# Kernel tuning notes

Hardware: AMD Instinct MI355X
Metric: run time of the kernel (lower is better)

The kernel has to match this reference:

```python
import jax, jax.numpy as jnp
import numpy as np

H = 1152      # embed_dim
NH = 16       # num heads
HD = H // NH  # head_dim = 72
SCALE = HD ** -0.5
B, S = 16, 729


def fake_quant(x, bits):
    """Symmetric per-tensor fake quantize-dequantize with straight-through estimator."""
    qmax = 2.0 ** (bits - 1) - 1.0
    scale = jnp.maximum(jnp.max(jnp.abs(x)), 1e-8) / qmax
    q = jnp.clip(jnp.round(x / scale), -qmax - 1.0, qmax) * scale
    return x + jax.lax.stop_gradient(q - x)  # STE


def fq_linear(x, W, b):
    # FakeQuantLinear: 8-bit fake-quant on activations and weights, fp accumulate
    return fake_quant(x, 8) @ fake_quant(W, 8).T + b


def setup_inputs() -> dict:
    key = jax.random.key(0)
    ks = jax.random.split(key, 9)
    std = H ** -0.5
    return {
        "hidden_states": jax.random.normal(ks[0], (B, S, H), jnp.float32),
        "Wq": jax.random.normal(ks[1], (H, H), jnp.float32) * std,
        "bq": jax.random.normal(ks[2], (H,), jnp.float32) * 0.02,
        "Wk": jax.random.normal(ks[3], (H, H), jnp.float32) * std,
        "bk": jax.random.normal(ks[4], (H,), jnp.float32) * 0.02,
        "Wv": jax.random.normal(ks[5], (H, H), jnp.float32) * std,
        "bv": jax.random.normal(ks[6], (H,), jnp.float32) * 0.02,
        "Wo": jax.random.normal(ks[7], (H, H), jnp.float32) * std,
        "bo": jax.random.normal(ks[8], (H,), jnp.float32) * 0.02,
    }


def reference(hidden_states, Wq, bq, Wk, bk, Wv, bv, Wo, bo):
    b, s, _ = hidden_states.shape
    q = fq_linear(hidden_states, Wq, bq).reshape(b, s, NH, HD).transpose(0, 2, 1, 3)
    k = fq_linear(hidden_states, Wk, bk).reshape(b, s, NH, HD).transpose(0, 2, 1, 3)
    v = fq_linear(hidden_states, Wv, bv).reshape(b, s, NH, HD).transpose(0, 2, 1, 3)
    # FakeQuantMatmul(8, 16): 8-bit quant on both matmul inputs, 16-bit quant on output
    attn = fake_quant(
        jnp.einsum("bhqd,bhkd->bhqk", fake_quant(q, 8), fake_quant(k, 8)), 16
    ) * SCALE
    # FakeQuantSoftmax(quant_bits=16): softmax then 16-bit fake quant
    attn = fake_quant(jax.nn.softmax(attn, axis=-1), 16)
    # FakeQuantMatmul(None, 8): no input quant, 8-bit output quant
    out = fake_quant(jnp.einsum("bhqk,bhkd->bhqd", attn, v), 8)
    out = out.transpose(0, 2, 1, 3).reshape(b, s, H)
    return fq_linear(out, Wo, bo)
```

## Files before the change

### kernel.cpp

```cpp
#include <hip/hip_runtime.h>
#include <math.h>

#define Hdim 1152
#define NHd  16
#define HDd  72
#define Bd   16
#define Sd   729
#define Ntok (Bd*Sd)
#define BHd  (Bd*NHd)
#define SCALE_F 0.117851130197757934f
#define LOG2E 1.44269504088896340736f

#define KFTB 8192
#define VFT 10240

#define SL_X 0
#define SL_WQ 1
#define SL_WK 2
#define SL_WV 3
#define SL_WO 4
#define SL_Q 5
#define SL_K 6
#define SL_LOGIT 8
#define SL_LMIN 9
#define SL_O 10

typedef short short8 __attribute__((ext_vector_type(8)));
typedef short short4v __attribute__((ext_vector_type(4)));
typedef float f32x4 __attribute__((ext_vector_type(4)));
typedef int int4v __attribute__((ext_vector_type(4)));

static __device__ __forceinline__ unsigned short f2bf(float f) {
  unsigned b = __float_as_uint(f);
  return (unsigned short)((b + 0x7FFFu + ((b >> 16) & 1u)) >> 16);
}
static __device__ __forceinline__ float bf2f(unsigned short u) {
  return __uint_as_float(((unsigned)u) << 16);
}
static __device__ __forceinline__ void atomicMaxF(float* p, float v) {
  atomicMax((unsigned int*)p, __float_as_uint(v));
}
static __device__ __forceinline__ void atomicMinF(float* p, float v) {
  atomicMin((unsigned int*)p, __float_as_uint(v));
}
static __device__ __forceinline__ float qscale(float mx, float qmax) {
  return fmaxf(mx, 1e-8f) / qmax;
}
static __device__ __forceinline__ float fexp2(float x) {
  float r; asm("v_exp_f32 %0, %1" : "=v"(r) : "v"(x)); return r;
}
static __device__ __forceinline__ float flog2(float x) {
  float r; asm("v_log_f32 %0, %1" : "=v"(r) : "v"(x)); return r;
}
static __device__ __forceinline__ short4v pack4(unsigned a, unsigned b, unsigned c, unsigned d) {
  union { unsigned u[2]; short4v s; } t;
  t.u[0] = a | (b << 16);
  t.u[1] = c | (d << 16);
  return t.s;
}
static __device__ __forceinline__ int q8i(float v, float s) {
  return (int)fminf(fmaxf(rintf(v / s), -128.f), 127.f);
}

#if __has_builtin(__builtin_amdgcn_mfma_f32_16x16x16bf16_1k)
#define MFMA16(a, b, c) __builtin_amdgcn_mfma_f32_16x16x16bf16_1k(a, b, c, 0, 0, 0)
#else
static __device__ __forceinline__ f32x4 MFMA16(short4v a, short4v b, f32x4 c) {
  asm("v_mfma_f32_16x16x16_bf16 %0, %1, %2, %0" : "+v"(c) : "v"(a), "v"(b));
  return c;
}
#endif
#if __has_builtin(__builtin_amdgcn_mfma_i32_16x16x64_i8)
#define MFMAI8(a, b, c) __builtin_amdgcn_mfma_i32_16x16x64_i8(a, b, c, 0, 0, 0)
#else
static __device__ __forceinline__ int4v MFMAI8(int4v a, int4v b, int4v c) {
  asm("v_mfma_i32_16x16x64_i8 %0, %1, %2, %0" : "+v"(c) : "v"(a), "v"(b));
  return c;
}
#endif

static __device__ __forceinline__ void gll16(const void* g, void* l) {
  __builtin_amdgcn_global_load_lds((const __attribute__((address_space(1))) void*)g,
                                   (__attribute__((address_space(3))) void*)l, 16, 0, 0);
}

__global__ void k_init(float* slots) {
  int i = threadIdx.x;
  if (i < 32) slots[i] = (i == SL_LMIN) ? __builtin_inff() : 0.0f;
}

__launch_bounds__(256)
__global__ void k_absmax(const float* __restrict__ X, const float* __restrict__ W0,
                         const float* __restrict__ W1, const float* __restrict__ W2,
                         const float* __restrict__ W3, float* slots) {
  int seg = blockIdx.y;
  const float* p; long n; int slot;
  if (seg == 0) { p = X; n = (long)Ntok * Hdim; slot = SL_X; }
  else {
    const float* ws4[4] = {W0, W1, W2, W3};
    p = ws4[seg - 1]; n = (long)Hdim * Hdim; slot = SL_WQ + seg - 1;
  }
  long n4 = n >> 2;
  const float4* p4 = (const float4*)p;
  float m = 0.f;
  for (long i = (long)blockIdx.x * blockDim.x + threadIdx.x; i < n4;
       i += (long)gridDim.x * blockDim.x) {
    float4 v = p4[i];
    m = fmaxf(m, fmaxf(fmaxf(fabsf(v.x), fabsf(v.y)), fmaxf(fabsf(v.z), fabsf(v.w))));
  }
  for (int off = 32; off; off >>= 1) m = fmaxf(m, __shfl_xor(m, off, 64));
  __shared__ float red[4];
  if ((threadIdx.x & 63) == 0) red[threadIdx.x >> 6] = m;
  __syncthreads();
  if (threadIdx.x == 0)
    atomicMaxF(&slots[slot], fmaxf(fmaxf(red[0], red[1]), fmaxf(red[2], red[3])));
}

__launch_bounds__(256)
__global__ void k_quant8i(const float* __restrict__ in, unsigned int* __restrict__ out,
                          long n, const float* __restrict__ slots, int slot) {
  float s = qscale(slots[slot], 127.0f);
  long n4 = n >> 2;
  const float4* in4 = (const float4*)in;
  for (long i = (long)blockIdx.x * blockDim.x + threadIdx.x; i < n4;
       i += (long)gridDim.x * blockDim.x) {
    float4 v = in4[i];
    unsigned a = (unsigned)q8i(v.x, s) & 255u;
    unsigned b = (unsigned)q8i(v.y, s) & 255u;
    unsigned c = (unsigned)q8i(v.z, s) & 255u;
    unsigned d = (unsigned)q8i(v.w, s) & 255u;
    out[i] = a | (b << 8) | (c << 16) | (d << 24);
  }
}

__launch_bounds__(256)
__global__ void k_quant8wi(const float* __restrict__ W0, const float* __restrict__ W1,
                           const float* __restrict__ W2, const float* __restrict__ W3,
                           unsigned int* O0, unsigned int* O1,
                           unsigned int* O2, unsigned int* O3,
                           const float* __restrict__ slots) {
  int seg = blockIdx.y;
  const float* ws4[4] = {W0, W1, W2, W3};
  unsigned int* os4[4] = {O0, O1, O2, O3};
  const float* in = ws4[seg];
  unsigned int* out = os4[seg];
  float s = qscale(slots[SL_WQ + seg], 127.0f);
  long n4 = ((long)Hdim * Hdim) >> 2;
  const float4* in4 = (const float4*)in;
  for (long i = (long)blockIdx.x * blockDim.x + threadIdx.x; i < n4;
       i += (long)gridDim.x * blockDim.x) {
    float4 v = in4[i];
    unsigned a = (unsigned)q8i(v.x, s) & 255u;
    unsigned b = (unsigned)q8i(v.y, s) & 255u;
    unsigned c = (unsigned)q8i(v.z, s) & 255u;
    unsigned d = (unsigned)q8i(v.w, s) & 255u;
    out[i] = a | (b << 8) | (c << 16) | (d << 24);
  }
}

#define GBM 128
#define GBN 128
#define GBK 64
__launch_bounds__(256, 3)
__global__ void k_gemm(const char* __restrict__ A,
                       const char* __restrict__ Bm,
                       const float* __restrict__ bias,
                       float* __restrict__ C,
                       float* slots, int slotA, int slotB, int slotOut) {
  __shared__ char As[GBM][GBK];
  __shared__ char Bs[GBN][GBK];
  __shared__ float red[4];
  int tid = threadIdx.x, lane = tid & 63, wid = tid >> 6;
  int wm = wid >> 1, wn = wid & 1;
  int l15 = lane & 15, l4 = lane >> 4;
  int bM = blockIdx.x, bN = blockIdx.y;
  int4v acc[4][4];
  for (int rf = 0; rf < 4; ++rf)
    for (int cf = 0; cf < 4; ++cf) acc[rf][cf] = int4v{0, 0, 0, 0};

  int srow = lane >> 2, scol = (lane & 3) * 16;
  const char* pa = A + ((long)(bM * GBM + wid * 32) + srow) * Hdim + scol;
  const char* pb = Bm + ((long)(bN * GBN + wid * 32) + srow) * Hdim + scol;

  for (int kt = 0; kt < Hdim / GBK; ++kt) {
    int kb = kt * GBK;
    __syncthreads();
    gll16(pa + kb, &As[wid * 32][0]);
    gll16(pa + kb + 16 * Hdim, &As[wid * 32 + 16][0]);
    gll16(pb + kb, &Bs[wid * 32][0]);
    gll16(pb + kb + 16 * Hdim, &Bs[wid * 32 + 16][0]);
    __syncthreads();
    int4v af[4], bf4[4];
#pragma unroll
    for (int rf = 0; rf < 4; ++rf) af[rf] = *(const int4v*)&As[wm * 64 + rf * 16 + l15][l4 * 16];
#pragma unroll
    for (int cf = 0; cf < 4; ++cf) bf4[cf] = *(const int4v*)&Bs[wn * 64 + cf * 16 + l15][l4 * 16];
#pragma unroll
    for (int rf = 0; rf < 4; ++rf)
#pragma unroll
      for (int cf = 0; cf < 4; ++cf)
        acc[rf][cf] = MFMAI8(af[rf], bf4[cf], acc[rf][cf]);
  }
  float alpha = qscale(slots[slotA], 127.f) * qscale(slots[slotB], 127.f);
  float lmax = 0.f;
#pragma unroll
  for (int cf = 0; cf < 4; ++cf) {
    int col = bN * GBN + wn * 64 + cf * 16 + l15;
    float bv = bias[col];
#pragma unroll
    for (int rf = 0; rf < 4; ++rf)
#pragma unroll
      for (int j = 0; j < 4; ++j) {
        int row = bM * GBM + wm * 64 + rf * 16 + l4 * 4 + j;
        if (row < Ntok) {
          float v = (float)acc[rf][cf][j] * alpha + bv;
          C[(long)row * Hdim + col] = v;
          lmax = fmaxf(lmax, fabsf(v));
        }
      }
  }
  if (slotOut >= 0) {
    for (int off = 32; off; off >>= 1) lmax = fmaxf(lmax, __shfl_xor(lmax, off, 64));
    if ((tid & 63) == 0) red[wid] = lmax;
    __syncthreads();
    if (tid == 0)
      atomicMaxF(&slots[slotOut], fmaxf(fmaxf(red[0], red[1]), fmaxf(red[2], red[3])));
  }
}

__launch_bounds__(256, 3)
__global__ void k_gemm3(const char* __restrict__ A,
                        const char* __restrict__ W0,
                        const char* __restrict__ W1,
                        const char* __restrict__ W2,
                        const float* __restrict__ b0, const float* __restrict__ b1,
                        const float* __restrict__ b2,
                        float* __restrict__ C0, float* __restrict__ C1,
                        float* __restrict__ C2, float* slots) {
  __shared__ char As[GBM][GBK];
  __shared__ char Bs[GBN][GBK];
  __shared__ float red[4];
  int bNg = blockIdx.y;
  int mi = bNg / 9, bN = bNg - mi * 9;
  const char* Bm = mi == 0 ? W0 : (mi == 1 ? W1 : W2);
  const float* bias = mi == 0 ? b0 : (mi == 1 ? b1 : b2);
  float* C = mi == 0 ? C0 : (mi == 1 ? C1 : C2);
  int slotB = SL_WQ + mi;
  int slotOut = mi == 0 ? SL_Q : (mi == 1 ? SL_K : -1);

  int tid = threadIdx.x, lane = tid & 63, wid = tid >> 6;
  int wm = wid >> 1, wn = wid & 1;
  int l15 = lane & 15, l4 = lane >> 4;
  int bM = blockIdx.x;
  int4v acc[4][4];
  for (int rf = 0; rf < 4; ++rf)
    for (int cf = 0; cf < 4; ++cf) acc[rf][cf] = int4v{0, 0, 0, 0};

  int srow = lane >> 2, scol = (lane & 3) * 16;
  const char* pa = A + ((long)(bM * GBM + wid * 32) + srow) * Hdim + scol;
  const char* pb = Bm + ((long)(bN * GBN + wid * 32) + srow) * Hdim + scol;

  for (int kt = 0; kt < Hdim / GBK; ++kt) {
    int kb = kt * GBK;
    __syncthreads();
    gll16(pa + kb, &As[wid * 32][0]);
    gll16(pa + kb + 16 * Hdim, &As[wid * 32 + 16][0]);
    gll16(pb + kb, &Bs[wid * 32][0]);
    gll16(pb + kb + 16 * Hdim, &Bs[wid * 32 + 16][0]);
    __syncthreads();
    int4v af[4], bf4[4];
#pragma unroll
    for (int rf = 0; rf < 4; ++rf) af[rf] = *(const int4v*)&As[wm * 64 + rf * 16 + l15][l4 * 16];
#pragma unroll
    for (int cf = 0; cf < 4; ++cf) bf4[cf] = *(const int4v*)&Bs[wn * 64 + cf * 16 + l15][l4 * 16];
#pragma unroll
    for (int rf = 0; rf < 4; ++rf)
#pragma unroll
      for (int cf = 0; cf < 4; ++cf)
        acc[rf][cf] = MFMAI8(af[rf], bf4[cf], acc[rf][cf]);
  }
  float alpha = qscale(slots[SL_X], 127.f) * qscale(slots[slotB], 127.f);
  float lmax = 0.f;
#pragma unroll
  for (int cf = 0; cf < 4; ++cf) {
    int col = bN * GBN + wn * 64 + cf * 16 + l15;
    float bv = bias[col];
#pragma unroll
    for (int rf = 0; rf < 4; ++rf)
#pragma unroll
      for (int j = 0; j < 4; ++j) {
        int row = bM * GBM + wm * 64 + rf * 16 + l4 * 4 + j;
        if (row < Ntok) {
          float v = (float)acc[rf][cf][j] * alpha + bv;
          C[(long)row * Hdim + col] = v;
          lmax = fmaxf(lmax, fabsf(v));
        }
      }
  }
  if (slotOut >= 0) {
    for (int off = 32; off; off >>= 1) lmax = fmaxf(lmax, __shfl_xor(lmax, off, 64));
    if ((tid & 63) == 0) red[wid] = lmax;
    __syncthreads();
    if (tid == 0)
      atomicMaxF(&slots[slotOut], fmaxf(fmaxf(red[0], red[1]), fmaxf(red[2], red[3])));
  }
}

__launch_bounds__(256)
__global__ void k_kfrag(const float* __restrict__ Kf, char* __restrict__ KF,
                        const float* __restrict__ slots) {
  int kt = blockIdx.x, bh = blockIdx.y;
  int b = bh >> 4, h = bh & 15;
  float s = qscale(slots[SL_K], 127.0f);
  int tid = threadIdx.x, lane = tid & 63, w = tid >> 6;
  int l15 = lane & 15, l4 = lane >> 4;
  long obase = ((long)(bh * 12 + kt)) * KFTB;
#pragma unroll
  for (int i = 0; i < 2; ++i) {
    int p = w * 2 + i;
    int cf = p >> 1, c = p & 1;
    int token = kt * 64 + cf * 16 + l15;
    char ov[16];
#pragma unroll
    for (int j = 0; j < 16; ++j) ov[j] = 0;
    if (token < Sd) {
      const float* src = &Kf[((long)(b * Sd + token)) * Hdim + h * HDd];
      if (c == 0) {
#pragma unroll
        for (int j = 0; j < 16; ++j) ov[j] = (char)q8i(src[l4 * 16 + j], s);
      } else if (l4 == 0) {
#pragma unroll
        for (int j = 0; j < 8; ++j) ov[j] = (char)q8i(src[64 + j], s);
      }
    }
    *(int4v*)&KF[obase + p * 1024 + lane * 16] = *(int4v*)ov;
  }
}

__launch_bounds__(256)
__global__ void k_vsplit(const float* __restrict__ Vf, unsigned short* __restrict__ VF) {
  int kt = blockIdx.x, bh = blockIdx.y;
  int b = bh >> 4, h = bh & 15;
  int tid = threadIdx.x, lane = tid & 63, w = tid >> 6;
  int l15 = lane & 15, l4 = lane >> 4;
  long obase = ((long)(bh * 12 + kt)) * VFT;
#pragma unroll
  for (int i = 0; i < 5; ++i) {
    int p = w + 4 * i;
    int dt = p >> 2, cf = p & 3;
    int d = dt * 16 + l15;
    int tok0 = kt * 64 + cf * 16 + l4 * 4;
    unsigned short u[8];
#pragma unroll
    for (int j = 0; j < 4; ++j) {
      int tok = tok0 + j;
      float v = 0.f;
      if (tok < Sd && d < HDd)
        v = Vf[((long)(b * Sd + tok)) * Hdim + h * HDd + d];
      unsigned short hb = f2bf(v);
      u[j] = hb;
      u[4 + j] = f2bf(v - bf2f(hb));
    }
    *(short8*)&VF[obase + (long)p * 512 + lane * 8] = *(short8*)u;
  }
}

static __device__ __forceinline__ void loadQ8(const char* __restrict__ Qq,
                                              int b, int h, int qc, int l4,
                                              int4v& qa, int4v& qb) {
  const char* qp = &Qq[((long)(b * Sd + qc)) * Hdim + h * HDd];
  union { long l[2]; int4v v; } u0, u1;
  u0.l[0] = *(const long*)(qp + l4 * 16);
  u0.l[1] = *(const long*)(qp + l4 * 16 + 8);
  qa = u0.v;
  u1.l[0] = (l4 == 0) ? *(const long*)(qp + 64) : 0L;
  u1.l[1] = 0L;
  qb = u1.v;
}

__launch_bounds__(256, 4)
__global__ void k_attnA(const char* __restrict__ Qq,
                        const char* __restrict__ KF, float* slots) {
  __shared__ float red[4];
  int qh = blockIdx.x, bh = blockIdx.y;
  int b = bh >> 4, h = bh & 15;
  int tid = threadIdx.x, lane = tid & 63, w = tid >> 6;
  int l15 = lane & 15, l4 = lane >> 4;
  const char* kfb = KF + (long)bh * 12 * KFTB;
  int4v qa[3], qb[3];
#pragma unroll
  for (int qs = 0; qs < 3; ++qs) {
    int qrow = (qh * 3 + qs) * 64 + w * 16 + l15;
    int qc = qrow > Sd - 1 ? Sd - 1 : qrow;
    loadQ8(Qq, b, h, qc, l4, qa[qs], qb[qs]);
  }
  float mx = 0.f;
#pragma unroll 1
  for (int kt = 0; kt < 12; ++kt) {
    int4v kf[8];
#pragma unroll
    for (int p = 0; p < 8; ++p)
      kf[p] = *(const int4v*)&kfb[(long)kt * KFTB + p * 1024 + lane * 16];
#pragma unroll
    for (int qs = 0; qs < 3; ++qs) {
#pragma unroll
      for (int cf = 0; cf < 4; ++cf) {
        int4v a = int4v{0, 0, 0, 0};
        a = MFMAI8(kf[cf * 2 + 0], qa[qs], a);
        a = MFMAI8(kf[cf * 2 + 1], qb[qs], a);
#pragma unroll
        for (int j = 0; j < 4; ++j) mx = fmaxf(mx, fabsf((float)a[j]));
      }
    }
  }
  mx *= qscale(slots[SL_Q], 127.f) * qscale(slots[SL_K], 127.f);
  for (int off = 32; off; off >>= 1) mx = fmaxf(mx, __shfl_xor(mx, off, 64));
  if ((tid & 63) == 0) red[w] = mx;
  __syncthreads();
  if (tid == 0)
    atomicMaxF(&slots[SL_LOGIT], fmaxf(fmaxf(red[0], red[1]), fmaxf(red[2], red[3])));
}

__launch_bounds__(256, 4)
__global__ void k_attnB(const char* __restrict__ Qq,
                        const char* __restrict__ KF, float* slots,
                        float* __restrict__ m_arr, float* __restrict__ l_arr) {
  __shared__ float red[4];
  int qh = blockIdx.x, bh = blockIdx.y;
  int b = bh >> 4, h = bh & 15;
  int tid = threadIdx.x, lane = tid & 63, w = tid >> 6;
  int l15 = lane & 15, l4 = lane >> 4;
  const char* kfb = KF + (long)bh * 12 * KFTB;
  int4v qa[3], qb[3];
#pragma unroll
  for (int qs = 0; qs < 3; ++qs) {
    int qrow = (qh * 3 + qs) * 64 + w * 16 + l15;
    int qc = qrow > Sd - 1 ? Sd - 1 : qrow;
    loadQ8(Qq, b, h, qc, l4, qa[qs], qb[qs]);
  }
  float s16 = qscale(slots[SL_LOGIT], 32767.f);
  float sqk = qscale(slots[SL_Q], 127.f) * qscale(slots[SL_K], 127.f);
  float c0 = sqk / s16;
  float c1e = s16 * SCALE_F * LOG2E;
  float m_run[3] = {-3.0e38f, -3.0e38f, -3.0e38f};
  float l_run[3] = {0.f, 0.f, 0.f};
#pragma unroll 1
  for (int kt = 0; kt < 12; ++kt) {
    int4v kf[8];
#pragma unroll
    for (int p = 0; p < 8; ++p)
      kf[p] = *(const int4v*)&kfb[(long)kt * KFTB + p * 1024 + lane * 16];
#pragma unroll
    for (int qs = 0; qs < 3; ++qs) {
      float nv[16];
#pragma unroll
      for (int cf = 0; cf < 4; ++cf) {
        int4v a = int4v{0, 0, 0, 0};
        a = MFMAI8(kf[cf * 2 + 0], qa[qs], a);
        a = MFMAI8(kf[cf * 2 + 1], qb[qs], a);
#pragma unroll
        for (int j = 0; j < 4; ++j) nv[cf * 4 + j] = rintf((float)a[j] * c0);
      }
      if (kt == 11) {
#pragma unroll
        for (int cf = 0; cf < 4; ++cf)
#pragma unroll
          for (int j = 0; j < 4; ++j) {
            int kcol = 704 + cf * 16 + l4 * 4 + j;
            if (kcol > Sd - 1) nv[cf * 4 + j] = -3.0e30f;
          }
      }
      float mt = nv[0];
#pragma unroll
      for (int i = 1; i < 16; ++i) mt = fmaxf(mt, nv[i]);
      mt = fmaxf(mt, __shfl_xor(mt, 16, 64));
      mt = fmaxf(mt, __shfl_xor(mt, 32, 64));
      float mn = fmaxf(m_run[qs], mt);
      float f = fexp2((m_run[qs] - mn) * c1e);
      float se = 0.f;
#pragma unroll
      for (int i = 0; i < 16; ++i) se += fexp2((nv[i] - mn) * c1e);
      se += __shfl_xor(se, 16, 64);
      se += __shfl_xor(se, 32, 64);
      l_run[qs] = l_run[qs] * f + se;
      m_run[qs] = mn;
    }
  }
  float lmin = 3.0e38f;
#pragma unroll
  for (int qs = 0; qs < 3; ++qs) {
    int qrow = (qh * 3 + qs) * 64 + w * 16 + l15;
    if (qrow < Sd) {
      if (l4 == 0) {
        m_arr[bh * Sd + qrow] = m_run[qs];
        l_arr[bh * Sd + qrow] = l_run[qs];
      }
      lmin = fminf(lmin, l_run[qs]);
    }
  }
  for (int off = 32; off; off >>= 1) lmin = fminf(lmin, __shfl_xor(lmin, off, 64));
  if ((tid & 63) == 0) red[w] = lmin;
  __syncthreads();
  if (tid == 0)
    atomicMinF(&slots[SL_LMIN], fminf(fminf(red[0], red[1]), fminf(red[2], red[3])));
}

__launch_bounds__(256, 5)
__global__ void k_attnC(const char* __restrict__ Qq,
                        const char* __restrict__ KF,
                        const unsigned short* __restrict__ VF,
                        const float* __restrict__ m_arr, const float* __restrict__ l_arr,
                        float* slots, float* __restrict__ O) {
  __shared__ char Ks[KFTB];
  __shared__ unsigned short Vs[VFT];
  __shared__ float red[4];
  int qp, bh;
  {
    int id = blockIdx.y * 6 + blockIdx.x;
    int xcd = id & 7, sub = id >> 3;
    int bhl = sub / 6;
    qp = sub - bhl * 6;
    bh = xcd * 32 + bhl;
  }
  int b = bh >> 4, h = bh & 15;
  int tid = threadIdx.x, lane = tid & 63, w = tid >> 6;
  int l15 = lane & 15, l4 = lane >> 4;
  float s16 = qscale(slots[SL_LOGIT], 32767.f);
  float sqk = qscale(slots[SL_Q], 127.f) * qscale(slots[SL_K], 127.f);
  float c0 = sqk / s16;
  float c1e = s16 * SCALE_F * LOG2E;
  float pmaxv = 1.0f / slots[SL_LMIN];
  float sp = fmaxf(pmaxv, 1e-8f) / 32767.0f;
  float inv_sp = 1.0f / sp;
  int4v qa[2], qb[2];
  float dexp[2];
#pragma unroll
  for (int qs = 0; qs < 2; ++qs) {
    int qrow = (qp * 2 + qs) * 64 + w * 16 + l15;
    int qc = qrow > Sd - 1 ? Sd - 1 : qrow;
    loadQ8(Qq, b, h, qc, l4, qa[qs], qb[qs]);
    float mn = m_arr[bh * Sd + qc];
    float c2 = (1.0f / l_arr[bh * Sd + qc]) * inv_sp;
    dexp[qs] = flog2(c2) - mn * c1e;
  }
  const char* kfb = KF + (long)bh * 12 * KFTB;
  const unsigned short* vfb = VF + (long)bh * 12 * VFT;
  f32x4 acc[2][5];
#pragma unroll
  for (int qs = 0; qs < 2; ++qs)
#pragma unroll
    for (int i = 0; i < 5; ++i) acc[qs][i] = f32x4{0.f, 0.f, 0.f, 0.f};

#pragma unroll 1
  for (int kt = 0; kt < 12; ++kt) {
    __syncthreads();
    {
      const char* kg = kfb + (long)kt * KFTB;
#pragma unroll
      for (int i = 0; i < 2; ++i) {
        int c = w * 2 + i;
        gll16(kg + c * 1024 + lane * 16, &Ks[c * 1024]);
      }
      const unsigned short* vg = vfb + (long)kt * VFT;
#pragma unroll
      for (int i = 0; i < 5; ++i) {
        int c = w + 4 * i;
        gll16(vg + c * 512 + lane * 8, &Vs[c * 512]);
      }
    }
    __syncthreads();
#pragma unroll
    for (int cf = 0; cf < 4; ++cf) {
      int4v k0 = *(const int4v*)&Ks[(cf * 2 + 0) * 1024 + lane * 16];
      int4v k1 = *(const int4v*)&Ks[(cf * 2 + 1) * 1024 + lane * 16];
      short4v Pp[2], Pr[2];
#pragma unroll
      for (int qs = 0; qs < 2; ++qs) {
        int4v a = int4v{0, 0, 0, 0};
        a = MFMAI8(k0, qa[qs], a);
        a = MFMAI8(k1, qb[qs], a);
        unsigned phb[4], rsb[4];
#pragma unroll
        for (int j = 0; j < 4; ++j) {
          float n = rintf((float)a[j] * c0);
          float nn = rintf(fexp2(fmaf(n, c1e, dexp[qs])));
          unsigned ub = __float_as_uint(nn);
          unsigned ph = (ub + 0x7FFFu + ((ub >> 16) & 1u)) >> 16;
          float rsf = nn - __uint_as_float(ph << 16);
          phb[j] = ph;
          rsb[j] = __float_as_uint(rsf) >> 16;
        }
        Pp[qs] = pack4(phb[0], phb[1], phb[2], phb[3]);
        Pr[qs] = pack4(rsb[0], rsb[1], rsb[2], rsb[3]);
      }
#pragma unroll
      for (int dt = 0; dt < 5; ++dt) {
        short8 vv = *(const short8*)&Vs[(dt * 4 + cf) * 512 + lane * 8];
        short4v vh = __builtin_shufflevector(vv, vv, 0, 1, 2, 3);
        short4v vl = __builtin_shufflevector(vv, vv, 4, 5, 6, 7);
#pragma unroll
        for (int qs = 0; qs < 2; ++qs) {
          acc[qs][dt] = MFMA16(Pp[qs], vh, acc[qs][dt]);
          acc[qs][dt] = MFMA16(Pp[qs], vl, acc[qs][dt]);
          acc[qs][dt] = MFMA16(Pr[qs], vh, acc[qs][dt]);
        }
      }
    }
  }
  float lmax = 0.f;
#pragma unroll
  for (int qs = 0; qs < 2; ++qs)
#pragma unroll
    for (int dt = 0; dt < 5; ++dt) {
      int d = dt * 16 + l15;
#pragma unroll
      for (int j = 0; j < 4; ++j) {
        int qr = (qp * 2 + qs) * 64 + w * 16 + l4 * 4 + j;
        if (qr < Sd && d < HDd) {
          float v = sp * acc[qs][dt][j];
          O[((long)(b * Sd + qr)) * Hdim + h * HDd + d] = v;
          lmax = fmaxf(lmax, fabsf(v));
        }
      }
    }
  for (int off = 32; off; off >>= 1) lmax = fmaxf(lmax, __shfl_xor(lmax, off, 64));
  if ((tid & 63) == 0) red[w] = lmax;
  __syncthreads();
  if (tid == 0)
    atomicMaxF(&slots[SL_O], fmaxf(fmaxf(red[0], red[1]), fmaxf(red[2], red[3])));
}

extern "C" void kernel_launch(void* const* d_in, const int* in_sizes, int n_in,
                              void* d_out, int out_size, void* d_ws, size_t ws_size,
                              hipStream_t stream) {
  const float* Xin = (const float*)d_in[0];
  const float* Wq = (const float*)d_in[1];
  const float* bq = (const float*)d_in[2];
  const float* Wk = (const float*)d_in[3];
  const float* bk = (const float*)d_in[4];
  const float* Wv = (const float*)d_in[5];
  const float* bv = (const float*)d_in[6];
  const float* Wo = (const float*)d_in[7];
  const float* bo = (const float*)d_in[8];
  float* out = (float*)d_out;
  char* ws = (char*)d_ws;

  size_t off = 0;
  auto alloc = [&](size_t bytes) {
    void* p = ws + off;
    off = (off + bytes + 255) & ~(size_t)255;
    return p;
  };
  float* slots = (float*)alloc(256);
  char* Xq  = (char*)alloc((size_t)Ntok * Hdim);
  char* Wqq = (char*)alloc((size_t)Hdim * Hdim);
  char* Wkq = (char*)alloc((size_t)Hdim * Hdim);
  char* Wvq = (char*)alloc((size_t)Hdim * Hdim);
  char* Woq = (char*)alloc((size_t)Hdim * Hdim);
  float* Kf = (float*)alloc((size_t)Ntok * Hdim * 4);
  float* Vf = (float*)alloc((size_t)Ntok * Hdim * 4);
  char* Qq = (char*)alloc((size_t)Ntok * Hdim);
  char* KFr = (char*)alloc((size_t)BHd * 12 * KFTB);
  unsigned short* VFr = (unsigned short*)alloc((size_t)BHd * 12 * VFT * 2);
  float* m_arr = (float*)alloc((size_t)BHd * Sd * 4);
  float* l_arr = (float*)alloc((size_t)BHd * Sd * 4);
  char* Oq = (char*)Vf;
  float* Qf = out;
  float* Of = out;

  k_init<<<1, 64, 0, stream>>>(slots);
  k_absmax<<<dim3(256, 5), 256, 0, stream>>>(Xin, Wq, Wk, Wv, Wo, slots);
  k_quant8i<<<1024, 256, 0, stream>>>(Xin, (unsigned int*)Xq, (long)Ntok * Hdim, slots, SL_X);
  k_quant8wi<<<dim3(128, 4), 256, 0, stream>>>(Wq, Wk, Wv, Wo, (unsigned int*)Wqq,
                                               (unsigned int*)Wkq, (unsigned int*)Wvq,
                                               (unsigned int*)Woq, slots);

  k_gemm3<<<dim3(92, 27), 256, 0, stream>>>(Xq, Wqq, Wkq, Wvq, bq, bk, bv,
                                            Qf, Kf, Vf, slots);

  k_quant8i<<<1024, 256, 0, stream>>>(Qf, (unsigned int*)Qq, (long)Ntok * Hdim, slots, SL_Q);
  k_kfrag<<<dim3(12, 256), 256, 0, stream>>>(Kf, KFr, slots);
  k_vsplit<<<dim3(12, 256), 256, 0, stream>>>(Vf, VFr);

  k_attnA<<<dim3(4, 256), 256, 0, stream>>>(Qq, KFr, slots);
  k_attnB<<<dim3(4, 256), 256, 0, stream>>>(Qq, KFr, slots, m_arr, l_arr);
  k_attnC<<<dim3(6, 256), 256, 0, stream>>>(Qq, KFr, VFr, m_arr, l_arr, slots, Of);

  k_quant8i<<<1024, 256, 0, stream>>>(Of, (unsigned int*)Oq, (long)Ntok * Hdim, slots, SL_O);
  k_gemm<<<dim3(92, 9), 256, 0, stream>>>(Oq, Woq, bo, out, slots, SL_O, SL_WO, -1);
}
```

Before: 491.0 us.

## Double GEMM K-step per barrier, XOR-swizzle LDS, truncate bf16 split in attention

New measurement: 468.2 us. -4.6%, faster.

```diff
diff --git a/kernel.cpp b/kernel.cpp
--- a/kernel.cpp
+++ b/kernel.cpp
@@ -160,15 +160,59 @@
 
 #define GBM 128
 #define GBN 128
-#define GBK 64
+static __device__ __forceinline__ void gemm_core(const char* __restrict__ A,
+                                                 const char* __restrict__ Bm,
+                                                 int bM, int bN, int tid,
+                                                 char (*As)[GBM][64],
+                                                 char (*Bs)[GBN][64],
+                                                 int4v acc[4][4]) {
+  int lane = tid & 63, wid = tid >> 6;
+  int wm = wid >> 1, wn = wid & 1;
+  int l15 = lane & 15, l4 = lane >> 4;
+  int srow = lane >> 2;
+  int scol = ((lane & 3) ^ ((lane >> 3) & 3)) * 16;
+  const char* pa = A + ((long)(bM * GBM + wid * 32) + srow) * Hdim + scol;
+  const char* pb = Bm + ((long)(bN * GBN + wid * 32) + srow) * Hdim + scol;
+  int csw = (l4 ^ ((l15 >> 1) & 3)) * 16;
+
+  for (int kt = 0; kt < 9; ++kt) {
+    int kb = kt * 128;
+    __syncthreads();
+    gll16(pa + kb,                 &As[0][wid * 32][0]);
+    gll16(pa + kb + 16 * Hdim,     &As[0][wid * 32 + 16][0]);
+    gll16(pa + kb + 64,            &As[1][wid * 32][0]);
+    gll16(pa + kb + 64 + 16 * Hdim,&As[1][wid * 32 + 16][0]);
+    gll16(pb + kb,                 &Bs[0][wid * 32][0]);
+    gll16(pb + kb + 16 * Hdim,     &Bs[0][wid * 32 + 16][0]);
+    gll16(pb + kb + 64,            &Bs[1][wid * 32][0]);
+    gll16(pb + kb + 64 + 16 * Hdim,&Bs[1][wid * 32 + 16][0]);
+    __syncthreads();
+#pragma unroll
+    for (int t = 0; t < 2; ++t) {
+      int4v af[4], bf4[4];
+#pragma unroll
+      for (int rf = 0; rf < 4; ++rf)
+        af[rf] = *(const int4v*)&As[t][wm * 64 + rf * 16 + l15][csw];
+#pragma unroll
+      for (int cf = 0; cf < 4; ++cf)
+        bf4[cf] = *(const int4v*)&Bs[t][wn * 64 + cf * 16 + l15][csw];
+#pragma unroll
+      for (int rf = 0; rf < 4; ++rf)
+#pragma unroll
+        for (int cf = 0; cf < 4; ++cf)
+          acc[rf][cf] = MFMAI8(af[rf], bf4[cf], acc[rf][cf]);
+    }
+  }
+}
+
 __launch_bounds__(256, 3)
 __global__ void k_gemm(const char* __restrict__ A,
                        const char* __restrict__ Bm,
                        const float* __restrict__ bias,
                        float* __restrict__ C,
                        float* slots, int slotA, int slotB, int slotOut) {
-  __shared__ char As[GBM][GBK];
-  __shared__ char Bs[GBN][GBK];
+  __shared__ char As[2][GBM][64];
+  __shared__ char Bs[2][GBN][64];
   __shared__ float red[4];
   int tid = threadIdx.x, lane = tid & 63, wid = tid >> 6;
   int wm = wid >> 1, wn = wid & 1;
@@ -177,30 +221,7 @@
   int4v acc[4][4];
   for (int rf = 0; rf < 4; ++rf)
     for (int cf = 0; cf < 4; ++cf) acc[rf][cf] = int4v{0, 0, 0, 0};
-
-  int srow = lane >> 2, scol = (lane & 3) * 16;
-  const char* pa = A + ((long)(bM * GBM + wid * 32) + srow) * Hdim + scol;
-  const char* pb = Bm + ((long)(bN * GBN + wid * 32) + srow) * Hdim + scol;
-
-  for (int kt = 0; kt < Hdim / GBK; ++kt) {
-    int kb = kt * GBK;
-    __syncthreads();
-    gll16(pa + kb, &As[wid * 32][0]);
-    gll16(pa + kb + 16 * Hdim, &As[wid * 32 + 16][0]);
-    gll16(pb + kb, &Bs[wid * 32][0]);
-    gll16(pb + kb + 16 * Hdim, &Bs[wid * 32 + 16][0]);
-    __syncthreads();
-    int4v af[4], bf4[4];
-#pragma unroll
-    for (int rf = 0; rf < 4; ++rf) af[rf] = *(const int4v*)&As[wm * 64 + rf * 16 + l15][l4 * 16];
-#pragma unroll
-    for (int cf = 0; cf < 4; ++cf) bf4[cf] = *(const int4v*)&Bs[wn * 64 + cf * 16 + l15][l4 * 16];
-#pragma unroll
-    for (int rf = 0; rf < 4; ++rf)
-#pragma unroll
-      for (int cf = 0; cf < 4; ++cf)
-        acc[rf][cf] = MFMAI8(af[rf], bf4[cf], acc[rf][cf]);
-  }
+  gemm_core(A, Bm, bM, bN, tid, As, Bs, acc);
   float alpha = qscale(slots[slotA], 127.f) * qscale(slots[slotB], 127.f);
   float lmax = 0.f;
 #pragma unroll
@@ -237,8 +258,8 @@
                         const float* __restrict__ b2,
                         float* __restrict__ C0, float* __restrict__ C1,
                         float* __restrict__ C2, float* slots) {
-  __shared__ char As[GBM][GBK];
-  __shared__ char Bs[GBN][GBK];
+  __shared__ char As[2][GBM][64];
+  __shared__ char Bs[2][GBN][64];
   __shared__ float red[4];
   int bNg = blockIdx.y;
   int mi = bNg / 9, bN = bNg - mi * 9;
@@ -255,30 +276,7 @@
   int4v acc[4][4];
   for (int rf = 0; rf < 4; ++rf)
     for (int cf = 0; cf < 4; ++cf) acc[rf][cf] = int4v{0, 0, 0, 0};
-
-  int srow = lane >> 2, scol = (lane & 3) * 16;
-  const char* pa = A + ((long)(bM * GBM + wid * 32) + srow) * Hdim + scol;
-  const char* pb = Bm + ((long)(bN * GBN + wid * 32) + srow) * Hdim + scol;
-
-  for (int kt = 0; kt < Hdim / GBK; ++kt) {
-    int kb = kt * GBK;
-    __syncthreads();
-    gll16(pa + kb, &As[wid * 32][0]);
-    gll16(pa + kb + 16 * Hdim, &As[wid * 32 + 16][0]);
-    gll16(pb + kb, &Bs[wid * 32][0]);
-    gll16(pb + kb + 16 * Hdim, &Bs[wid * 32 + 16][0]);
-    __syncthreads();
-    int4v af[4], bf4[4];
-#pragma unroll
-    for (int rf = 0; rf < 4; ++rf) af[rf] = *(const int4v*)&As[wm * 64 + rf * 16 + l15][l4 * 16];
-#pragma unroll
-    for (int cf = 0; cf < 4; ++cf) bf4[cf] = *(const int4v*)&Bs[wn * 64 + cf * 16 + l15][l4 * 16];
-#pragma unroll
-    for (int rf = 0; rf < 4; ++rf)
-#pragma unroll
-      for (int cf = 0; cf < 4; ++cf)
-        acc[rf][cf] = MFMAI8(af[rf], bf4[cf], acc[rf][cf]);
-  }
+  gemm_core(A, Bm, bM, bN, tid, As, Bs, acc);
   float alpha = qscale(slots[SL_X], 127.f) * qscale(slots[slotB], 127.f);
   float lmax = 0.f;
 #pragma unroll
@@ -585,9 +583,9 @@
           float n = rintf((float)a[j] * c0);
           float nn = rintf(fexp2(fmaf(n, c1e, dexp[qs])));
           unsigned ub = __float_as_uint(nn);
-          unsigned ph = (ub + 0x7FFFu + ((ub >> 16) & 1u)) >> 16;
-          float rsf = nn - __uint_as_float(ph << 16);
-          phb[j] = ph;
+          unsigned hb = ub & 0xFFFF0000u;
+          float rsf = nn - __uint_as_float(hb);
+          phb[j] = hb >> 16;
           rsb[j] = __float_as_uint(rsf) >> 16;
         }
         Pp[qs] = pack4(phb[0], phb[1], phb[2], phb[3]);
```
